# Optimization experiments

Measured on AMD Instinct MI355X. Metric: run time of the kernel, lower is better.

The kernel has to match this reference:

```python
import jax, jax.numpy as jnp
import numpy as np
from jax import lax

GROUPS = 32  # in_channels // reduction_ratio


def setup_inputs() -> dict:
    key = jax.random.key(0)
    ks = jax.random.split(key, 12)
    B, C, H, W = 4, 256, 64, 64
    Cr = C // 8  # 32
    s = lambda k, shape, sc: jax.random.normal(k, shape, dtype=jnp.float32) * sc
    return {
        "x": s(ks[0], (B, C, H, W), 1.0),
        "wq": s(ks[1], (C, C), 0.05),          # 1x1 query conv + folded BN
        "bq": s(ks[2], (C,), 0.05),
        "wv": s(ks[3], (C, C), 0.05),          # 1x1 value conv + folded BN
        "bv": s(ks[4], (C,), 0.05),
        "w_adj1": s(ks[5], (Cr, C // GROUPS, 3), 0.1),   # grouped Conv1d OIH
        "b_adj1": s(ks[6], (Cr,), 0.05),
        "w_adj2": s(ks[7], (2 * Cr, Cr, 3), 0.1),        # Conv1d + folded BN1d
        "b_adj2": s(ks[8], (2 * Cr,), 0.05),
        "gamma": s(ks[9], (1,), 1.0),
        "w_co": s(ks[10], (C, C // 2, 4, 4), 0.05),      # ConvTranspose2d IOHW
        "b_co": s(ks[11], (C // 2,), 0.05),
    }


def reference(x, wq, bq, wv, bv, w_adj1, b_adj1, w_adj2, b_adj2, gamma, w_co, b_co):
    B, C, H, W = x.shape
    HW = H * W
    dn1 = ("NCH", "OIH", "NCH")

    # query path: 1x1 conv (+BN folded) -> [B, C, HW]
    q = jnp.einsum("oc,bchw->bohw", wq, x).reshape(B, C, HW) + bq[None, :, None]
    # conv_adj: grouped Conv1d k=3 p=1, then Conv1d k=3 p=1 (+BN1d folded)
    q = lax.conv_general_dilated(q, w_adj1, (1,), ((1, 1),),
                                 dimension_numbers=dn1,
                                 feature_group_count=GROUPS) + b_adj1[None, :, None]
    q = lax.conv_general_dilated(q, w_adj2, (1,), ((1, 1),),
                                 dimension_numbers=dn1) + b_adj2[None, :, None]
    q = q.reshape(B, C // 8, 2, HW)  # [B, Cr, 2, HW]
    query_y = q[:, :, 0, :]          # [B, Cr, HW]
    key_y = q[:, :, 1, :]            # [B, Cr, HW]

    # attention: [B, HW, HW]
    attn = jnp.einsum("bcn,bcm->bnm", query_y, key_y)
    attn_f = jax.nn.softmax(attn, axis=0)  # softmax over BATCH (faithful to source)
    attn_b = jax.nn.softmax(attn, axis=1)  # softmax over first HW axis

    # value path
    value = jnp.einsum("oc,bchw->bohw", wv, x).reshape(B, C, HW) + bv[None, :, None]

    # fusion[b,c,n] = sum_m value[b,c,m] * attn[b,n,m]
    fusion = jnp.einsum("bcm,bnm->bcn", value, attn_f + attn_b)
    fusion = gamma * fusion

    # AdaptiveAvgPool2d(1) on the 3D [B,C,HW] tensor == global mean per batch sample
    spatial = jnp.mean(x, axis=(1, 2, 3))  # [B]
    fusion = fusion * spatial[:, None, None]

    fusion = fusion.reshape(B, C, H, W) + x

    # ConvTranspose2d(C, C//2, k=4, s=2, p=1): flip kernel, swap I/O, input-dilated conv
    wt = jnp.flip(w_co, (2, 3)).transpose(1, 0, 2, 3)  # [out, in, 4, 4]
    out = lax.conv_general_dilated(fusion, wt, (1, 1), ((2, 2), (2, 2)),
                                   lhs_dilation=(2, 2),
                                   dimension_numbers=("NCHW", "OIHW", "NCHW"))
    out = out + b_co[None, :, None, None]  # [B, C//2, 2H, 2W]
    return out
```

## Files before the change

### kernel.cpp

```cpp
#include <hip/hip_runtime.h>

#define BN 4
#define CC 256
#define NN 4096
#define CR 32
#define OCH 128
#define SEGS 8

typedef float f32x4 __attribute__((ext_vector_type(4)));
typedef short short8 __attribute__((ext_vector_type(8)));
typedef unsigned short u16x8 __attribute__((ext_vector_type(8)));
typedef unsigned short u16x4 __attribute__((ext_vector_type(4)));

__device__ __forceinline__ unsigned short f2b(float f) {
  unsigned u = __builtin_bit_cast(unsigned, f);
  u += 0x7fff + ((u >> 16) & 1);
  return (unsigned short)(u >> 16);
}
__device__ __forceinline__ float b2f(unsigned short h) {
  unsigned u = ((unsigned)h) << 16;
  return __builtin_bit_cast(float, u);
}

__global__ __launch_bounds__(256) void k_wcast(const float* __restrict__ wq,
    const float* __restrict__ wv, unsigned short* __restrict__ wqb,
    unsigned short* __restrict__ wvb) {
  const int gid = (blockIdx.x * 256 + threadIdx.x) * 4;
  const float* src = blockIdx.y ? wv : wq;
  unsigned short* dst = blockIdx.y ? wvb : wqb;
  const float4 v = *(const float4*)(src + gid);
  u16x4 o; o[0] = f2b(v.x); o[1] = f2b(v.y); o[2] = f2b(v.z); o[3] = f2b(v.w);
  *(u16x4*)(dst + gid) = o;
}

__global__ __launch_bounds__(256) void k_xt(const float* __restrict__ x,
    unsigned short* __restrict__ xt, float* __restrict__ part2) {
  __shared__ unsigned short T[64][65];
  __shared__ float red[256];
  const int b = blockIdx.z, c0 = blockIdx.y * 64, n0 = blockIdx.x * 64;
  const int t = threadIdx.x;
  float s = 0.f;
  for (int idx = t; idx < 4096; idx += 256) {
    int i = idx >> 6, j = idx & 63;
    const float v = x[((size_t)(b * CC + c0 + i)) * NN + n0 + j];
    s += v;
    T[i][j] = f2b(v);
  }
  __syncthreads();
  for (int idx = t; idx < 4096; idx += 256) {
    int j = idx >> 6, i = idx & 63;
    xt[((size_t)(b * NN + n0 + j)) * CC + c0 + i] = T[i][j];
  }
  red[t] = s;
  __syncthreads();
  for (int d = 128; d > 0; d >>= 1) {
    if (t < d) red[t] += red[t + d];
    __syncthreads();
  }
  if (t == 0) part2[b * 256 + blockIdx.y * 64 + blockIdx.x] = red[0];
}

__global__ void k_spatial2(const float* __restrict__ part2, float* __restrict__ spatial) {
  const int b = blockIdx.x;
  const int t = threadIdx.x;
  __shared__ float red[256];
  red[t] = part2[b * 256 + t];
  __syncthreads();
  for (int d = 128; d > 0; d >>= 1) {
    if (t < d) red[t] += red[t + d];
    __syncthreads();
  }
  if (t == 0) spatial[b] = red[0] * (1.0f / ((float)CC * NN));
}

__global__ __launch_bounds__(256) void k_projm(const unsigned short* __restrict__ xt,
    const unsigned short* __restrict__ wqb, const float* __restrict__ bq,
    const unsigned short* __restrict__ wvb, const float* __restrict__ bv,
    unsigned short* __restrict__ q1b, unsigned short* __restrict__ Vb) {
  const int b = blockIdx.y, n0 = blockIdx.x * 32, which = blockIdx.z;
  const unsigned short* W = which ? wvb : wqb;
  const float* bias = which ? bv : bq;
  unsigned short* out = which ? Vb : q1b;
  const int t = threadIdx.x;
  const int w = t >> 6, l = t & 63;
  const int lo = l & 15, hi = l >> 4;
  const int oc0 = w * 64;
  f32x4 acc[4][2];
#pragma unroll
  for (int ct = 0; ct < 4; ++ct)
#pragma unroll
    for (int nt = 0; nt < 2; ++nt) acc[ct][nt] = (f32x4){0.f, 0.f, 0.f, 0.f};
  const unsigned short* wb = W + (size_t)(oc0 + lo) * CC + hi * 8;
  const unsigned short* xb = xt + ((size_t)(b * NN + n0 + lo)) * CC + hi * 8;
#pragma unroll
  for (int k0 = 0; k0 < CC; k0 += 32) {
    short8 aw[4], bx[2];
#pragma unroll
    for (int ct = 0; ct < 4; ++ct) aw[ct] = *(const short8*)(wb + ct * 16 * CC + k0);
#pragma unroll
    for (int nt = 0; nt < 2; ++nt) bx[nt] = *(const short8*)(xb + nt * 16 * CC + k0);
#pragma unroll
    for (int ct = 0; ct < 4; ++ct)
#pragma unroll
      for (int nt = 0; nt < 2; ++nt)
        acc[ct][nt] = __builtin_amdgcn_mfma_f32_16x16x32_bf16(aw[ct], bx[nt], acc[ct][nt], 0, 0, 0);
  }
#pragma unroll
  for (int ct = 0; ct < 4; ++ct) {
#pragma unroll
    for (int r = 0; r < 4; ++r) {
      const int c = oc0 + ct * 16 + hi * 4 + r;
      const float bvv = bias[c];
#pragma unroll
      for (int nt = 0; nt < 2; ++nt)
        out[((size_t)(b * CC + c)) * NN + n0 + nt * 16 + lo] = f2b(acc[ct][nt][r] + bvv);
    }
  }
}

__global__ __launch_bounds__(256) void k_adj1(const unsigned short* __restrict__ q1,
    const float* __restrict__ w1, const float* __restrict__ b1,
    float* __restrict__ q2) {
  const int gid = blockIdx.x * 256 + threadIdx.x;
  const int n8 = gid & 511;
  const int o = (gid >> 9) & 31;
  const int b = gid >> 14;
  const int n0 = n8 * 8;
  const unsigned short* base = q1 + ((size_t)b * CC + o * 8) * NN;
  float accv[8];
  const float bias = b1[o];
#pragma unroll
  for (int j = 0; j < 8; ++j) accv[j] = bias;
#pragma unroll
  for (int i = 0; i < 8; ++i) {
    const unsigned short* r = base + (size_t)i * NN;
    const u16x8 v = *(const u16x8*)(r + n0);
    float f[10];
    f[0] = (n0 > 0) ? b2f(r[n0 - 1]) : 0.f;
#pragma unroll
    for (int j = 0; j < 8; ++j) f[j + 1] = b2f(v[j]);
    f[9] = (n0 + 8 < NN) ? b2f(r[n0 + 8]) : 0.f;
    const float wa = w1[o * 24 + i * 3 + 0];
    const float wb = w1[o * 24 + i * 3 + 1];
    const float wc = w1[o * 24 + i * 3 + 2];
#pragma unroll
    for (int j = 0; j < 8; ++j) accv[j] += wa * f[j] + wb * f[j + 1] + wc * f[j + 2];
  }
  float4* dst = (float4*)&q2[((size_t)b * CR + o) * NN + n0];
  dst[0] = make_float4(accv[0], accv[1], accv[2], accv[3]);
  dst[1] = make_float4(accv[4], accv[5], accv[6], accv[7]);
}

__global__ __launch_bounds__(256) void k_adj2(const float* __restrict__ q2,
    const float* __restrict__ w2, const float* __restrict__ b2,
    unsigned short* __restrict__ Qt, unsigned short* __restrict__ Kt) {
  __shared__ float q2s[32][66];
  __shared__ float w2t[96][64];
  __shared__ float b2s[64];
  const int b = blockIdx.y, n0 = blockIdx.x * 64;
  const int t = threadIdx.x;
  for (int idx = t; idx < 32 * 66; idx += 256) {
    int c = idx / 66, nn = idx % 66;
    int n = n0 + nn - 1;
    q2s[c][nn] = (n >= 0 && n < NN) ? q2[((size_t)b * CR + c) * NN + n] : 0.f;
  }
  for (int idx = t; idx < 96 * 64; idx += 256) {
    int k = idx & 63, ct = idx >> 6;
    w2t[ct][k] = w2[k * 96 + ct];
  }
  if (t < 64) b2s[t] = b2[t];
  __syncthreads();
  const int nn = t & 63, kh = t >> 6;
  float acc[16];
#pragma unroll
  for (int i = 0; i < 16; ++i) acc[i] = b2s[kh * 16 + i];
  for (int c = 0; c < 32; ++c) {
    const float x0 = q2s[c][nn], x1 = q2s[c][nn + 1], x2 = q2s[c][nn + 2];
    const float* wa = &w2t[c * 3 + 0][kh * 16];
    const float* wb = &w2t[c * 3 + 1][kh * 16];
    const float* wc = &w2t[c * 3 + 2][kh * 16];
#pragma unroll
    for (int i = 0; i < 16; ++i)
      acc[i] += wa[i] * x0 + wb[i] * x1 + wc[i] * x2;
  }
  const size_t row = ((size_t)b * NN + n0 + nn) * 32;
  u16x8 qo, ko;
#pragma unroll
  for (int i = 0; i < 8; ++i) {
    qo[i] = f2b(acc[2 * i] * 1.44269504f);
    ko[i] = f2b(acc[2 * i + 1]);
  }
  *(u16x8*)(Qt + row + kh * 8) = qo;
  *(u16x8*)(Kt + row + kh * 8) = ko;
}

__global__ __launch_bounds__(512) void k_colstatm(const unsigned short* __restrict__ Qt,
    const unsigned short* __restrict__ Kt, float* __restrict__ psum) {
  __shared__ float CS[2][4][64];
  const int m0 = blockIdx.x * 64, seg = blockIdx.y;
  const int t = threadIdx.x;
  const int w = t >> 6, l = t & 63;
  const int lo = l & 15, hi = l >> 4;
  const int mt = w & 3, nt2 = w >> 2;
  const f32x4 zero4 = (f32x4){0.f, 0.f, 0.f, 0.f};
  short8 kf[4];
#pragma unroll
  for (int bb = 0; bb < 4; ++bb)
    kf[bb] = *(const short8*)(Kt + ((size_t)(bb * NN + m0 + mt * 16 + lo)) * 32 + hi * 8);
  float colacc[4] = {0.f, 0.f, 0.f, 0.f};
  for (int ch = 0; ch < 8; ++ch) {
    const int nb = seg * 512 + ch * 64;
    short8 qf[2][4];
#pragma unroll
    for (int pos = 0; pos < 2; ++pos)
#pragma unroll
      for (int bb = 0; bb < 4; ++bb)
        qf[pos][bb] = *(const short8*)(Qt + ((size_t)(bb * NN + nb + (nt2 * 2 + pos) * 16 + lo)) * 32 + hi * 8);
#pragma unroll
    for (int pos = 0; pos < 2; ++pos) {
#pragma unroll
      for (int bb = 0; bb < 4; ++bb) {
        const f32x4 s = __builtin_amdgcn_mfma_f32_16x16x32_bf16(qf[pos][bb], kf[bb], zero4, 0, 0, 0);
#pragma unroll
        for (int r = 0; r < 4; ++r) colacc[bb] += __builtin_amdgcn_exp2f(fminf(s[r], 86.f));
      }
    }
  }
#pragma unroll
  for (int bb = 0; bb < 4; ++bb) {
    colacc[bb] += __shfl_xor(colacc[bb], 16, 64);
    colacc[bb] += __shfl_xor(colacc[bb], 32, 64);
  }
  if (hi == 0) {
#pragma unroll
    for (int bb = 0; bb < 4; ++bb) CS[nt2][bb][mt * 16 + lo] = colacc[bb];
  }
  __syncthreads();
  if (t < 256) {
    const int bb = t >> 6, mm = t & 63;
    psum[((size_t)(bb * SEGS + seg)) * NN + m0 + mm] = CS[0][bb][mm] + CS[1][bb][mm];
  }
}

__global__ void k_rsum(const float* __restrict__ psum, float* __restrict__ rcs) {
  const int gid = blockIdx.x * 256 + threadIdx.x;
  const int b = gid >> 12, m = gid & (NN - 1);
  float S = 0.f;
#pragma unroll
  for (int s = 0; s < SEGS; ++s) S += psum[((size_t)(b * SEGS + s)) * NN + m];
  rcs[gid] = 1.0f / S;
}

__global__ __launch_bounds__(512) void k_aden(const unsigned short* __restrict__ Qt,
    const unsigned short* __restrict__ Kt, unsigned short* __restrict__ rden) {
  const int ntile = blockIdx.x, mseg = blockIdx.y;
  const int t = threadIdx.x;
  const int w = t >> 6, l = t & 63;
  const int lo = l & 15, hi = l >> 4;
  const int mt = w & 3, nh = w >> 2;
  const f32x4 zero4 = (f32x4){0.f, 0.f, 0.f, 0.f};
  short8 qf[4];
#pragma unroll
  for (int bb = 0; bb < 4; ++bb)
    qf[bb] = *(const short8*)(Qt + ((size_t)(bb * NN + ntile * 32 + nh * 16 + lo)) * 32 + hi * 8);
  const int slot = (mt * 2 + nh) * 64 + hi * 16 + lo;
  for (int ch = 0; ch < 8; ++ch) {
    const int m0 = mseg * 512 + ch * 64;
    short8 kf[4];
#pragma unroll
    for (int bb = 0; bb < 4; ++bb)
      kf[bb] = *(const short8*)(Kt + ((size_t)(bb * NN + m0 + mt * 16 + lo)) * 32 + hi * 8);
    f32x4 s[4];
#pragma unroll
    for (int bb = 0; bb < 4; ++bb)
      s[bb] = __builtin_amdgcn_mfma_f32_16x16x32_bf16(kf[bb], qf[bb], zero4, 0, 0, 0);
    u16x4 av;
#pragma unroll
    for (int r = 0; r < 4; ++r) {
      const float e0 = __builtin_amdgcn_exp2f(fminf(s[0][r], 86.f));
      const float e1 = __builtin_amdgcn_exp2f(fminf(s[1][r], 86.f));
      const float e2 = __builtin_amdgcn_exp2f(fminf(s[2][r], 86.f));
      const float e3 = __builtin_amdgcn_exp2f(fminf(s[3][r], 86.f));
      av[r] = f2b(__builtin_amdgcn_rcpf(e0 + e1 + e2 + e3));
    }
    *(u16x4*)(rden + ((size_t)(ntile * 64 + mseg * 8 + ch)) * 2048 + slot * 4) = av;
  }
}

__global__ __launch_bounds__(512, 6) void k_fused7(const unsigned short* __restrict__ Qt,
    const unsigned short* __restrict__ Kt, const unsigned short* __restrict__ Vb,
    const unsigned short* __restrict__ rden, const float* __restrict__ x,
    const float* __restrict__ rcs, const float* __restrict__ gamma,
    const float* __restrict__ spatial, unsigned short* __restrict__ fusb) {
  __shared__ unsigned short Pool[256 * 64 + 2 * 2304];
  unsigned short* VsB = Pool;
  unsigned short* AsB = Pool + 256 * 64;
  const int id = blockIdx.x;
  const int b = (id & 7) >> 1;
  const int ntile = ((id >> 3) << 1) | (id & 1);
  const int n0 = ntile * 32;
  const int t = threadIdx.x;
  const int w = t >> 6, l = t & 63;
  const int lo = l & 15, hi = l >> 4;
  const int mt = w & 3, ns = w >> 2;
  const f32x4 zero4 = (f32x4){0.f, 0.f, 0.f, 0.f};
  unsigned short* Vsw = VsB + w * 2048;

  const short8 qf = *(const short8*)(Qt + ((size_t)(b * NN + n0 + ns * 16 + lo)) * 32 + hi * 8);

  f32x4 acc[2][2];
#pragma unroll
  for (int ct = 0; ct < 2; ++ct)
#pragma unroll
    for (int nt = 0; nt < 2; ++nt) acc[ct][nt] = zero4;

  const int cl_base = l >> 3, jj = l & 7;
  const unsigned short* vwave = Vb + ((size_t)(b * CC + w * 32)) * NN;
  const unsigned short* kbase = Kt + ((size_t)(b * NN + mt * 16 + lo)) * 32 + hi * 8;
  const unsigned short* rdbase = rden + ((size_t)ntile * 64) * 2048
                               + (size_t)((mt * 2 + ns) * 64 + hi * 16 + lo) * 4;
  const float* rcs_b = rcs + b * NN;
  const int as_off = (ns * 16 + lo) * 72 + mt * 16 + hi * 4;

  short8 kf = *(const short8*)(kbase);
  {
    u16x8 vst[4];
#pragma unroll
    for (int q = 0; q < 4; ++q) {
      const int cl = q * 8 + cl_base;
      vst[q] = *(const u16x8*)(vwave + (size_t)cl * NN + jj * 8);
    }
    const u16x4 rd4 = *(const u16x4*)(rdbase);
    const f32x4 s = __builtin_amdgcn_mfma_f32_16x16x32_bf16(kf, qf, zero4, 0, 0, 0);
    const f32x4 rc4 = *(const f32x4*)(rcs_b + mt * 16 + hi * 4);
    u16x4 av;
#pragma unroll
    for (int r = 0; r < 4; ++r) {
      const float e = __builtin_amdgcn_exp2f(fminf(s[r], 86.f));
      av[r] = f2b(e * (b2f(rd4[r]) + rc4[r]));
    }
    *(u16x4*)&AsB[as_off] = av;
#pragma unroll
    for (int q = 0; q < 4; ++q) {
      const int cl = q * 8 + cl_base;
      *(u16x8*)&Vsw[cl * 64 + ((jj ^ (cl & 7)) << 3)] = vst[q];
    }
    kf = *(const short8*)(kbase + (size_t)64 * 32);
  }
  __syncthreads();

  for (int ch = 0; ch < 64; ++ch) {
    const int cur = ch & 1;
    unsigned short* Asc = AsB + cur * 2304;
    unsigned short* Asn = AsB + (cur ^ 1) * 2304;
    u16x8 vst[4];
    u16x4 av;
    if (ch < 63) {
      const int m1 = (ch + 1) * 64;
#pragma unroll
      for (int q = 0; q < 4; ++q) {
        const int cl = q * 8 + cl_base;
        vst[q] = *(const u16x8*)(vwave + (size_t)cl * NN + m1 + jj * 8);
      }
      const u16x4 rd4 = *(const u16x4*)(rdbase + (size_t)(ch + 1) * 2048);
      const f32x4 s = __builtin_amdgcn_mfma_f32_16x16x32_bf16(kf, qf, zero4, 0, 0, 0);
      const f32x4 rc4 = *(const f32x4*)(rcs_b + m1 + mt * 16 + hi * 4);
#pragma unroll
      for (int r = 0; r < 4; ++r) {
        const float e = __builtin_amdgcn_exp2f(fminf(s[r], 86.f));
        av[r] = f2b(e * (b2f(rd4[r]) + rc4[r]));
      }
      const int m2 = (ch < 62) ? (m1 + 64) : m1;
      kf = *(const short8*)(kbase + (size_t)m2 * 32);
    }
#pragma unroll
    for (int kt = 0; kt < 2; ++kt) {
      short8 af[2];
#pragma unroll
      for (int nt = 0; nt < 2; ++nt)
        af[nt] = *(const short8*)&Asc[(nt * 16 + lo) * 72 + kt * 32 + hi * 8];
#pragma unroll
      for (int ct = 0; ct < 2; ++ct) {
        const int cl = ct * 16 + lo;
        const short8 vf = *(const short8*)&Vsw[cl * 64 + (((kt * 4 + hi) ^ (cl & 7)) << 3)];
#pragma unroll
        for (int nt = 0; nt < 2; ++nt)
          acc[ct][nt] = __builtin_amdgcn_mfma_f32_16x16x32_bf16(vf, af[nt], acc[ct][nt], 0, 0, 0);
      }
    }
    if (ch < 63) {
#pragma unroll
      for (int q = 0; q < 4; ++q) {
        const int cl = q * 8 + cl_base;
        *(u16x8*)&Vsw[cl * 64 + ((jj ^ (cl & 7)) << 3)] = vst[q];
      }
      *(u16x4*)&Asn[as_off] = av;
    }
    __syncthreads();
  }

  unsigned short* Fs = Pool;
  const float g = gamma[0] * spatial[b];
#pragma unroll
  for (int ct = 0; ct < 2; ++ct) {
#pragma unroll
    for (int nt = 0; nt < 2; ++nt) {
      u16x4 o4;
#pragma unroll
      for (int r = 0; r < 4; ++r) {
        const int c = w * 32 + ct * 16 + hi * 4 + r;
        const float xv = x[((size_t)(b * CC + c)) * NN + n0 + nt * 16 + lo];
        o4[r] = f2b(g * acc[ct][nt][r] + xv);
      }
      *(u16x4*)&Fs[(nt * 16 + lo) * 264 + w * 32 + ct * 16 + hi * 4] = o4;
    }
  }
  __syncthreads();
  const int iy = n0 >> 6, ix0 = n0 & 63;
  unsigned short* fb = fusb + (((size_t)(b * 66 + iy + 1)) * 66 + ix0 + 1) * 256;
#pragma unroll
  for (int q = 0; q < 2; ++q) {
    const int u = t + q * 512;
    const int nl = u >> 5, c0 = (u & 31) * 8;
    *(u16x8*)(fb + (size_t)nl * 256 + c0) = *(const u16x8*)&Fs[nl * 264 + c0];
  }
}

__global__ void k_wprep(const float* __restrict__ w_co, unsigned short* __restrict__ wbf) {
  const int gid = blockIdx.x * 256 + threadIdx.x;
  const int ic = gid & 255;
  const int o = (gid >> 8) & 127;
  const int tap = (gid >> 15) & 3;
  const int p = gid >> 17;
  const int py = p >> 1, px = p & 1;
  const int tyi = tap >> 1, txi = tap & 1;
  const int ky = py + 2 * tyi, kx = px + 2 * txi;
  wbf[gid] = f2b(w_co[(ic * 128 + o) * 16 + (3 - ky) * 4 + (3 - kx)]);
}

__global__ __launch_bounds__(512) void k_deconv(const unsigned short* __restrict__ fusb,
    const unsigned short* __restrict__ wbf, const float* __restrict__ b_co,
    float* __restrict__ out) {
  __shared__ unsigned short Fsh[5 * 66 * 36];
  __shared__ unsigned short Wsh[4 * 128 * 36];
  const int bp = blockIdx.y;
  const int b = bp >> 2, py = (bp >> 1) & 1, px = bp & 1;
  const int t = threadIdx.x;
  const int w = t >> 6, l = t & 63;
  const int lo = l & 15, hi = l >> 4;
  const int wm = w & 1, wrow = w >> 1;
  const int iy0 = blockIdx.x * 4;
  const int iy = iy0 + wrow;
  f32x4 acc[4][4];
#pragma unroll
  for (int mt = 0; mt < 4; ++mt)
#pragma unroll
    for (int nt = 0; nt < 4; ++nt) acc[mt][nt] = (f32x4){0.f, 0.f, 0.f, 0.f};
  const unsigned short* wp_base = wbf + (size_t)(bp & 3) * 4 * 128 * 256;
  const size_t frow0 = (size_t)(b * 66 + iy0 + py) * 66;

  for (int ic0 = 0; ic0 < 256; ic0 += 32) {
    __syncthreads();
#pragma unroll
    for (int pass = 0; pass < 3; ++pass) {
      const int idx = t + pass * 512;
      if (idx < 1320) {
        const int rr = idx / 264, rem = idx % 264;
        const int xxp = rem >> 2, h = rem & 3;
        const u16x8 v = *(const u16x8*)(fusb + (frow0 + (size_t)rr * 66 + xxp) * 256 + ic0 + h * 8);
        *(u16x8*)&Fsh[(rr * 66 + xxp) * 36 + h * 8] = v;
      }
    }
#pragma unroll
    for (int pass = 0; pass < 4; ++pass) {
      const int idx = t + pass * 512;
      const int tap = idx >> 9, o = (idx >> 2) & 127, h = idx & 3;
      const u16x8 v = *(const u16x8*)(wp_base + (size_t)tap * 32768 + (size_t)o * 256 + ic0 + h * 8);
      *(u16x8*)&Wsh[(tap * 128 + o) * 36 + h * 8] = v;
    }
    __syncthreads();
#pragma unroll
    for (int tap = 0; tap < 4; ++tap) {
      const int tyi = tap >> 1, txi = tap & 1;
      const int dx = px + txi - 1;
      const int rr = wrow + tyi;
      short8 a[4], bf[4];
#pragma unroll
      for (int mt = 0; mt < 4; ++mt)
        a[mt] = *(const short8*)&Wsh[(tap * 128 + wm * 64 + mt * 16 + lo) * 36 + hi * 8];
#pragma unroll
      for (int nt = 0; nt < 4; ++nt)
        bf[nt] = *(const short8*)&Fsh[(rr * 66 + nt * 16 + lo + dx + 1) * 36 + hi * 8];
#pragma unroll
      for (int mt = 0; mt < 4; ++mt)
#pragma unroll
        for (int nt = 0; nt < 4; ++nt)
          acc[mt][nt] = __builtin_amdgcn_mfma_f32_16x16x32_bf16(a[mt], bf[nt], acc[mt][nt], 0, 0, 0);
    }
  }
  const int y = 2 * iy + py;
#pragma unroll
  for (int mt = 0; mt < 4; ++mt) {
#pragma unroll
    for (int nt = 0; nt < 4; ++nt) {
#pragma unroll
      for (int r = 0; r < 4; ++r) {
        const int o = wm * 64 + mt * 16 + hi * 4 + r;
        const int xx = 2 * (nt * 16 + lo) + px;
        out[(((size_t)(b * OCH + o)) * 128 + y) * 128 + xx] = acc[mt][nt][r] + b_co[o];
      }
    }
  }
}

extern "C" void kernel_launch(void* const* d_in, const int* in_sizes, int n_in,
                              void* d_out, int out_size, void* d_ws, size_t ws_size,
                              hipStream_t stream) {
  const float* x     = (const float*)d_in[0];
  const float* wq    = (const float*)d_in[1];
  const float* bq    = (const float*)d_in[2];
  const float* wv    = (const float*)d_in[3];
  const float* bv    = (const float*)d_in[4];
  const float* w1    = (const float*)d_in[5];
  const float* b1    = (const float*)d_in[6];
  const float* w2    = (const float*)d_in[7];
  const float* b2    = (const float*)d_in[8];
  const float* gamma = (const float*)d_in[9];
  const float* w_co  = (const float*)d_in[10];
  const float* b_co  = (const float*)d_in[11];
  float* out = (float*)d_out;
  (void)in_sizes; (void)n_in; (void)out_size; (void)ws_size;

  char* p = (char*)d_ws;
  unsigned short* xt      = (unsigned short*)p; p += (size_t)BN * NN * CC * 2;
  unsigned short* q1b     = (unsigned short*)p; p += (size_t)BN * CC * NN * 2;
  float*          q2      = (float*)p;          p += (size_t)BN * CR * NN * 4;
  float*          psum    = (float*)p;          p += (size_t)BN * SEGS * NN * 4;
  float*          part2   = (float*)p;          p += (size_t)1024 * 4;
  unsigned short* Qt      = (unsigned short*)p; p += (size_t)BN * NN * 32 * 2;
  unsigned short* Kt      = (unsigned short*)p; p += (size_t)BN * NN * 32 * 2;
  unsigned short* Vb      = (unsigned short*)p; p += (size_t)BN * CC * NN * 2;
  float*          rcs     = (float*)p;          p += (size_t)BN * NN * 4;
  float*          spatial = (float*)p;          p += 256;
  unsigned short* wqb     = (unsigned short*)p; p += (size_t)CC * CC * 2;
  unsigned short* wvb     = (unsigned short*)p; p += (size_t)CC * CC * 2;
  unsigned short* wbf     = (unsigned short*)p; p += (size_t)4 * 4 * 128 * 256 * 2;
  unsigned short* fusb    = (unsigned short*)p; p += (size_t)BN * 66 * 66 * 256 * 2;
  unsigned short* rden    = (unsigned short*)p; p += (size_t)NN * NN * 2;

  hipMemsetAsync(fusb, 0, (size_t)BN * 66 * 66 * 256 * 2, stream);

  k_wcast<<<dim3(64, 2), 256, 0, stream>>>(wq, wv, wqb, wvb);
  k_xt<<<dim3(64, 4, 4), 256, 0, stream>>>(x, xt, part2);
  k_projm<<<dim3(128, 4, 2), 256, 0, stream>>>(xt, wqb, bq, wvb, bv, q1b, Vb);
  k_adj1<<<dim3(256), 256, 0, stream>>>(q1b, w1, b1, q2);
  k_adj2<<<dim3(64, 4), 256, 0, stream>>>(q2, w2, b2, Qt, Kt);
  k_spatial2<<<dim3(4), 256, 0, stream>>>(part2, spatial);
  k_colstatm<<<dim3(64, SEGS), 512, 0, stream>>>(Qt, Kt, psum);
  k_rsum<<<dim3(64), 256, 0, stream>>>(psum, rcs);
  k_aden<<<dim3(128, 8), 512, 0, stream>>>(Qt, Kt, rden);
  k_wprep<<<dim3(2048), 256, 0, stream>>>(w_co, wbf);
  k_fused7<<<dim3(512), 512, 0, stream>>>(Qt, Kt, Vb, rden, x, rcs, gamma, spatial, fusb);
  k_deconv<<<dim3(16, 16), 512, 0, stream>>>(fusb, wbf, b_co, out);
}
```

Baseline: 219.0 us.

## Fuse batch-softmax denominator computation into column-statistics kernel

Removes the separate k_aden kernel and computes the per-element batch-softmax reciprocal denominators inside k_colstatm, reusing the same QK^T MFMA results and exp2 values already needed for the column sums. Results are staged through shared memory and written to rden in the tile layout k_fused7 expects. This drops one kernel launch and a full recomputation of the 4096x4096x4 score matmul and exponentials. In exchange it adds two block barriers per chunk in the column-stat loop and a remapped output layout that must match the old indexing exactly.

```diff
diff --git a/kernel.cpp b/kernel.cpp
--- a/kernel.cpp
+++ b/kernel.cpp
@@ -195,9 +195,12 @@
 }
 
 __global__ __launch_bounds__(512) void k_colstatm(const unsigned short* __restrict__ Qt,
-    const unsigned short* __restrict__ Kt, float* __restrict__ psum) {
+    const unsigned short* __restrict__ Kt, float* __restrict__ psum,
+    unsigned short* __restrict__ rden) {
   __shared__ float CS[2][4][64];
+  __shared__ unsigned short RD[2][2048];
   const int m0 = blockIdx.x * 64, seg = blockIdx.y;
+  const int bx = blockIdx.x;
   const int t = threadIdx.x;
   const int w = t >> 6, l = t & 63;
   const int lo = l & 15, hi = l >> 4;
@@ -208,23 +211,39 @@
   for (int bb = 0; bb < 4; ++bb)
     kf[bb] = *(const short8*)(Kt + ((size_t)(bb * NN + m0 + mt * 16 + lo)) * 32 + hi * 8);
   float colacc[4] = {0.f, 0.f, 0.f, 0.f};
+  const int rd_base = mt * 512 + (lo >> 2) * 64 + hi * 16 + (lo & 3);
   for (int ch = 0; ch < 8; ++ch) {
     const int nb = seg * 512 + ch * 64;
-    short8 qf[2][4];
-#pragma unroll
-    for (int pos = 0; pos < 2; ++pos)
+#pragma unroll
+    for (int pos = 0; pos < 2; ++pos) {
+      short8 qf[4];
 #pragma unroll
       for (int bb = 0; bb < 4; ++bb)
-        qf[pos][bb] = *(const short8*)(Qt + ((size_t)(bb * NN + nb + (nt2 * 2 + pos) * 16 + lo)) * 32 + hi * 8);
-#pragma unroll
-    for (int pos = 0; pos < 2; ++pos) {
-#pragma unroll
-      for (int bb = 0; bb < 4; ++bb) {
-        const f32x4 s = __builtin_amdgcn_mfma_f32_16x16x32_bf16(qf[pos][bb], kf[bb], zero4, 0, 0, 0);
-#pragma unroll
-        for (int r = 0; r < 4; ++r) colacc[bb] += __builtin_amdgcn_exp2f(fminf(s[r], 86.f));
-      }
-    }
+        qf[bb] = *(const short8*)(Qt + ((size_t)(bb * NN + nb + (nt2 * 2 + pos) * 16 + lo)) * 32 + hi * 8);
+      f32x4 s[4];
+#pragma unroll
+      for (int bb = 0; bb < 4; ++bb)
+        s[bb] = __builtin_amdgcn_mfma_f32_16x16x32_bf16(qf[bb], kf[bb], zero4, 0, 0, 0);
+      const int u = nt2 * 2 + pos;
+      unsigned short* rdp = &RD[u >> 1][(u & 1) * 256 + rd_base];
+#pragma unroll
+      for (int r = 0; r < 4; ++r) {
+        const float e0 = __builtin_amdgcn_exp2f(fminf(s[0][r], 86.f));
+        const float e1 = __builtin_amdgcn_exp2f(fminf(s[1][r], 86.f));
+        const float e2 = __builtin_amdgcn_exp2f(fminf(s[2][r], 86.f));
+        const float e3 = __builtin_amdgcn_exp2f(fminf(s[3][r], 86.f));
+        colacc[0] += e0; colacc[1] += e1; colacc[2] += e2; colacc[3] += e3;
+        rdp[r * 4] = f2b(__builtin_amdgcn_rcpf(e0 + e1 + e2 + e3));
+      }
+    }
+    __syncthreads();
+    {
+      const int uu = t * 8;
+      const int th = uu >> 11, off = uu & 2047;
+      const size_t gbase = ((size_t)((seg * 16 + ch * 2 + th) * 64 + bx)) * 2048;
+      *(u16x8*)(rden + gbase + off) = *(const u16x8*)&RD[th][off];
+    }
+    __syncthreads();
   }
 #pragma unroll
   for (int bb = 0; bb < 4; ++bb) {
@@ -249,42 +268,6 @@
 #pragma unroll
   for (int s = 0; s < SEGS; ++s) S += psum[((size_t)(b * SEGS + s)) * NN + m];
   rcs[gid] = 1.0f / S;
-}
-
-__global__ __launch_bounds__(512) void k_aden(const unsigned short* __restrict__ Qt,
-    const unsigned short* __restrict__ Kt, unsigned short* __restrict__ rden) {
-  const int ntile = blockIdx.x, mseg = blockIdx.y;
-  const int t = threadIdx.x;
-  const int w = t >> 6, l = t & 63;
-  const int lo = l & 15, hi = l >> 4;
-  const int mt = w & 3, nh = w >> 2;
-  const f32x4 zero4 = (f32x4){0.f, 0.f, 0.f, 0.f};
-  short8 qf[4];
-#pragma unroll
-  for (int bb = 0; bb < 4; ++bb)
-    qf[bb] = *(const short8*)(Qt + ((size_t)(bb * NN + ntile * 32 + nh * 16 + lo)) * 32 + hi * 8);
-  const int slot = (mt * 2 + nh) * 64 + hi * 16 + lo;
-  for (int ch = 0; ch < 8; ++ch) {
-    const int m0 = mseg * 512 + ch * 64;
-    short8 kf[4];
-#pragma unroll
-    for (int bb = 0; bb < 4; ++bb)
-      kf[bb] = *(const short8*)(Kt + ((size_t)(bb * NN + m0 + mt * 16 + lo)) * 32 + hi * 8);
-    f32x4 s[4];
-#pragma unroll
-    for (int bb = 0; bb < 4; ++bb)
-      s[bb] = __builtin_amdgcn_mfma_f32_16x16x32_bf16(kf[bb], qf[bb], zero4, 0, 0, 0);
-    u16x4 av;
-#pragma unroll
-    for (int r = 0; r < 4; ++r) {
-      const float e0 = __builtin_amdgcn_exp2f(fminf(s[0][r], 86.f));
-      const float e1 = __builtin_amdgcn_exp2f(fminf(s[1][r], 86.f));
-      const float e2 = __builtin_amdgcn_exp2f(fminf(s[2][r], 86.f));
-      const float e3 = __builtin_amdgcn_exp2f(fminf(s[3][r], 86.f));
-      av[r] = f2b(__builtin_amdgcn_rcpf(e0 + e1 + e2 + e3));
-    }
-    *(u16x4*)(rden + ((size_t)(ntile * 64 + mseg * 8 + ch)) * 2048 + slot * 4) = av;
-  }
 }
 
 __global__ __launch_bounds__(512, 6) void k_fused7(const unsigned short* __restrict__ Qt,
@@ -556,9 +539,8 @@
   k_adj1<<<dim3(256), 256, 0, stream>>>(q1b, w1, b1, q2);
   k_adj2<<<dim3(64, 4), 256, 0, stream>>>(q2, w2, b2, Qt, Kt);
   k_spatial2<<<dim3(4), 256, 0, stream>>>(part2, spatial);
-  k_colstatm<<<dim3(64, SEGS), 512, 0, stream>>>(Qt, Kt, psum);
+  k_colstatm<<<dim3(64, SEGS), 512, 0, stream>>>(Qt, Kt, psum, rden);
   k_rsum<<<dim3(64), 256, 0, stream>>>(psum, rcs);
-  k_aden<<<dim3(128, 8), 512, 0, stream>>>(Qt, Kt, rden);
   k_wprep<<<dim3(2048), 256, 0, stream>>>(w_co, wbf);
   k_fused7<<<dim3(512), 512, 0, stream>>>(Qt, Kt, Vb, rden, x, rcs, gamma, spatial, fusb);
   k_deconv<<<dim3(16, 16), 512, 0, stream>>>(fusb, wbf, b_co, out);
```

New measurement: 207.0 us. 1.06x faster.
